# Kernel optimization log

Measured on AMD Instinct MI355X. Metric: run time of the kernel, lower is better.

Reference implementation:

```python
import jax, jax.numpy as jnp
import numpy as np

EPS = 1e-12  # matches torch F.normalize default eps

def _l2_normalize(v, axis=-1):
    n = jnp.sqrt(jnp.sum(v * v, axis=axis, keepdims=True))
    return v / jnp.maximum(n, EPS)

def setup_inputs() -> dict:
    key = jax.random.key(0)
    k1, k2, k3 = jax.random.split(key, 3)
    B, S, D_IN, D_OUT, T = 4, 4096, 1024, 1024, 1024
    std = 1.0 / np.sqrt(D_IN)
    return {
        "x": jax.random.normal(k1, (B, S, D_IN), dtype=jnp.float32),
        "key_tokens": jax.random.normal(k2, (T, D_IN), dtype=jnp.float32) * std,
        "value_tokens": jax.random.normal(k3, (T, D_OUT), dtype=jnp.float32) * std,
        "temp": jnp.ones((T, 1), dtype=jnp.float32),
    }

def reference(x, key_tokens, value_tokens, temp):
    # x: [B,S,D_in]; key_tokens: [T,D_in]; value_tokens: [T,D_out]; temp: [T,1]
    x_norm = _l2_normalize(x)                      # [B,S,D_in]
    k_norm = _l2_normalize(key_tokens)             # [T,D_in]
    sim = jnp.einsum('bsd,td->bst', x_norm, k_norm)  # [B,S,T]
    sim = sim * jax.nn.sigmoid(temp).reshape(1, 1, -1)
    # mod_softmax: scale each row to RMS-norm sqrt(T), then exact GELU
    T = sim.shape[-1]
    scale = jnp.sqrt(jnp.float32(T)) / jnp.sqrt(jnp.sum(sim * sim, axis=-1, keepdims=True))
    weights = jax.nn.gelu(sim * scale, approximate=False)  # [B,S,T]
    return jnp.einsum('bst,to->bso', weights, value_tokens)  # [B,S,D_out]
```

## Files before the change

### kernel.cpp

```cpp
#include <hip/hip_runtime.h>
#include <math.h>

typedef __attribute__((ext_vector_type(8))) short short8;
typedef __attribute__((ext_vector_type(4))) float floatx4;

__device__ __forceinline__ float bf2f(unsigned short u) {
    union { unsigned int u; float f; } v;
    v.u = ((unsigned int)u) << 16;
    return v.f;
}

__device__ __forceinline__ unsigned short f2bf(float f) {
    union { float f; unsigned int u; } v;
    v.f = f;
    unsigned int r = v.u + 0x7fffu + ((v.u >> 16) & 1u);
    return (unsigned short)(r >> 16);
}

__device__ __forceinline__ void gload16_lds(const void* g, void* l) {
    __builtin_amdgcn_global_load_lds(
        (const __attribute__((address_space(1))) unsigned int*)g,
        (__attribute__((address_space(3))) unsigned int*)l, 16, 0, 0);
}

__device__ __forceinline__ ushort4 cvt4(float4 v, float fa) {
    ushort4 o;
    o.x = f2bf(v.x * fa); o.y = f2bf(v.y * fa);
    o.z = f2bf(v.z * fa); o.w = f2bf(v.w * fa);
    return o;
}

__global__ __launch_bounds__(256) void prep_kernel(
    const float* __restrict__ x, const float* __restrict__ key,
    const float* __restrict__ temp, const float* __restrict__ val,
    unsigned short* __restrict__ xb, unsigned short* __restrict__ kf,
    unsigned short* __restrict__ VT, float* __restrict__ rowsq,
    int M, int T, int D, int Dout, int nRowBlocks) {
    const int bid = blockIdx.x;
    if (bid < nRowBlocks) {
        const int lane = threadIdx.x & 63;
        const int nWaves = nRowBlocks << 2;
        const int totRows = M + T;
        for (int row = (bid << 2) | (int)(threadIdx.x >> 6); row < totRows;
             row += nWaves) {
            const bool isx = row < M;
            const int r = isx ? row : row - M;
            const float4* s4 =
                (const float4*)(isx ? (x + (size_t)r * D) : (key + (size_t)r * D));
            float4 v0 = s4[lane];
            float4 v1 = s4[lane + 64];
            float4 v2 = s4[lane + 128];
            float4 v3 = s4[lane + 192];
            float s = v0.x * v0.x + v0.y * v0.y + v0.z * v0.z + v0.w * v0.w;
            s += v1.x * v1.x + v1.y * v1.y + v1.z * v1.z + v1.w * v1.w;
            s += v2.x * v2.x + v2.y * v2.y + v2.z * v2.z + v2.w * v2.w;
            s += v3.x * v3.x + v3.y * v3.y + v3.z * v3.z + v3.w * v3.w;
#pragma unroll
            for (int o = 32; o > 0; o >>= 1) s += __shfl_xor(s, o, 64);
            float fa = 1.0f / fmaxf(sqrtf(s), 1e-12f);
            if (isx) {
                if (lane == 0) rowsq[r] = 0.0f;
            } else {
                fa = fa / (1.0f + expf(-temp[r]));
            }
            ushort4* dst =
                (ushort4*)(isx ? (xb + (size_t)r * D) : (kf + (size_t)r * D));
            dst[lane] = cvt4(v0, fa);
            dst[lane + 64] = cvt4(v1, fa);
            dst[lane + 128] = cvt4(v2, fa);
            dst[lane + 192] = cvt4(v3, fa);
        }
    } else {
        __shared__ unsigned short tile[64][65];
        const int idx = bid - nRowBlocks;
        const int nCt = Dout >> 6;
        const int c0 = (idx % nCt) * 64;
        const int r0 = (idx / nCt) * 64;
        const int t = threadIdx.x;
        for (int i = t; i < 4096; i += 256) {
            int rr = i >> 6, cc = i & 63;
            tile[rr][cc] = f2bf(val[(size_t)(r0 + rr) * Dout + c0 + cc]);
        }
        __syncthreads();
        for (int i = t; i < 4096; i += 256) {
            int rr = i >> 6, cc = i & 63;
            VT[(size_t)(c0 + rr) * T + r0 + cc] = tile[cc][rr];
        }
    }
}

template <int MODE>
__global__ __launch_bounds__(256, 2) void gemm_pipe(
    const unsigned short* __restrict__ A, const unsigned short* __restrict__ B,
    void* __restrict__ Cv, float* __restrict__ rowsq, int M, int N, int K) {
    __shared__ __align__(16) char smem[73728];
    const int tid = threadIdx.x;
    const int lane = tid & 63;
    const int w = tid >> 6;
    const int wr = w >> 1;
    const int wc = w & 1;
    const int m0 = blockIdx.x * 256;
    const int n0 = blockIdx.y * 128;
    const int q = lane >> 4;
    const int cl = lane & 15;

    const int srow = lane >> 2;
    const int sch = (lane & 3) ^ ((lane & 32) >> 4);
    const unsigned short* gA = A + (size_t)(m0 + w * 16 + srow) * K + sch * 8;
    const unsigned short* gB = B + (size_t)(n0 + w * 16 + srow) * K + sch * 8;
    const unsigned short* rA0 = gA;
    const unsigned short* rA1 = gA + (size_t)64 * K;
    const unsigned short* rA2 = gA + (size_t)128 * K;
    const unsigned short* rA3 = gA + (size_t)192 * K;
    const unsigned short* rB0 = gB;
    const unsigned short* rB1 = gB + (size_t)64 * K;

    char* stA = smem + w * 1024;
    char* stB = stA + 16384;

    const int LB = ((cl * 64 + q * 16) ^ ((lane & 8) << 2));
    const char* rdA = (const char*)smem + LB + wr * 8192;
    const char* rdB = (const char*)smem + LB + 16384 + wc * 4096;

    floatx4 acc[8][4];
#pragma unroll
    for (int i = 0; i < 8; i++)
#pragma unroll
        for (int j = 0; j < 4; j++) acc[i][j] = (floatx4){0.f, 0.f, 0.f, 0.f};

    short8 af0[4], af1[4], bf0[4], bf1[4];

    gload16_lds(rA0, stA);
    gload16_lds(rA1, stA + 4096);
    gload16_lds(rB0, stB);
    gload16_lds(rA2, stA + 8192);
    gload16_lds(rA3, stA + 12288);
    gload16_lds(rB1, stB + 4096);
    gload16_lds(rA0 + 32, stA + 24576);
    gload16_lds(rA1 + 32, stA + 24576 + 4096);
    gload16_lds(rB0 + 32, stB + 24576);
    gload16_lds(rA2 + 32, stA + 24576 + 8192);
    gload16_lds(rA3 + 32, stA + 24576 + 12288);
    gload16_lds(rB1 + 32, stB + 24576 + 4096);
    asm volatile("s_waitcnt vmcnt(6)" ::: "memory");
    __builtin_amdgcn_s_barrier();
    rA0 += 64; rA1 += 64; rA2 += 64; rA3 += 64; rB0 += 64; rB1 += 64;

#define MFMA16(AF, BF, RO)                                                   \
    _Pragma("unroll") for (int mt = 0; mt < 4; ++mt)                         \
        _Pragma("unroll") for (int nt = 0; nt < 4; ++nt)                     \
            acc[RO + mt][nt] = __builtin_amdgcn_mfma_f32_16x16x32_bf16(      \
                AF[mt], BF[nt], acc[RO + mt][nt], 0, 0, 0);

#define TILE(SLOT, SSLOT, BF, KOFF)                                          \
    {                                                                        \
        BF[0] = *(const short8*)(rdB + SLOT * 24576);                        \
        BF[1] = *(const short8*)(rdB + SLOT * 24576 + 1024);                 \
        BF[2] = *(const short8*)(rdB + SLOT * 24576 + 2048);                 \
        BF[3] = *(const short8*)(rdB + SLOT * 24576 + 3072);                 \
        af0[0] = *(const short8*)(rdA + SLOT * 24576);                       \
        af0[1] = *(const short8*)(rdA + SLOT * 24576 + 1024);                \
        af0[2] = *(const short8*)(rdA + SLOT * 24576 + 2048);                \
        af0[3] = *(const short8*)(rdA + SLOT * 24576 + 3072);                \
        gload16_lds(rA0 + KOFF, stA + SSLOT * 24576);                        \
        gload16_lds(rA1 + KOFF, stA + SSLOT * 24576 + 4096);                 \
        gload16_lds(rB0 + KOFF, stB + SSLOT * 24576);                        \
        __builtin_amdgcn_s_barrier();                                        \
        asm volatile("s_waitcnt lgkmcnt(0)" ::: "memory");                   \
        __builtin_amdgcn_sched_barrier(0);                                   \
        __builtin_amdgcn_s_setprio(1);                                       \
        MFMA16(af0, BF, 0)                                                   \
        __builtin_amdgcn_s_setprio(0);                                       \
        __builtin_amdgcn_s_barrier();                                        \
        af1[0] = *(const short8*)(rdA + SLOT * 24576 + 4096);                \
        af1[1] = *(const short8*)(rdA + SLOT * 24576 + 5120);                \
        af1[2] = *(const short8*)(rdA + SLOT * 24576 + 6144);                \
        af1[3] = *(const short8*)(rdA + SLOT * 24576 + 7168);                \
        gload16_lds(rA2 + KOFF, stA + SSLOT * 24576 + 8192);                 \
        gload16_lds(rA3 + KOFF, stA + SSLOT * 24576 + 12288);                \
        gload16_lds(rB1 + KOFF, stB + SSLOT * 24576 + 4096);                 \
        asm volatile("s_waitcnt vmcnt(6)" ::: "memory");                     \
        __builtin_amdgcn_s_barrier();                                        \
        asm volatile("s_waitcnt lgkmcnt(0)" ::: "memory");                   \
        __builtin_amdgcn_sched_barrier(0);                                   \
        __builtin_amdgcn_s_setprio(1);                                       \
        MFMA16(af1, BF, 4)                                                   \
        __builtin_amdgcn_s_setprio(0);                                       \
        __builtin_amdgcn_s_barrier();                                        \
    }

#define TILE_TAIL(SLOT, BF, DRAIN)                                           \
    {                                                                        \
        BF[0] = *(const short8*)(rdB + SLOT * 24576);                        \
        BF[1] = *(const short8*)(rdB + SLOT * 24576 + 1024);                 \
        BF[2] = *(const short8*)(rdB + SLOT * 24576 + 2048);                 \
        BF[3] = *(const short8*)(rdB + SLOT * 24576 + 3072);                 \
        af0[0] = *(const short8*)(rdA + SLOT * 24576);                       \
        af0[1] = *(const short8*)(rdA + SLOT * 24576 + 1024);                \
        af0[2] = *(const short8*)(rdA + SLOT * 24576 + 2048);                \
        af0[3] = *(const short8*)(rdA + SLOT * 24576 + 3072);                \
        __builtin_amdgcn_s_barrier();                                        \
        asm volatile("s_waitcnt lgkmcnt(0)" ::: "memory");                   \
        __builtin_amdgcn_sched_barrier(0);                                   \
        __builtin_amdgcn_s_setprio(1);                                       \
        MFMA16(af0, BF, 0)                                                   \
        __builtin_amdgcn_s_setprio(0);                                       \
        __builtin_amdgcn_s_barrier();                                        \
        af1[0] = *(const short8*)(rdA + SLOT * 24576 + 4096);                \
        af1[1] = *(const short8*)(rdA + SLOT * 24576 + 5120);                \
        af1[2] = *(const short8*)(rdA + SLOT * 24576 + 6144);                \
        af1[3] = *(const short8*)(rdA + SLOT * 24576 + 7168);                \
        if (DRAIN) asm volatile("s_waitcnt vmcnt(0)" ::: "memory");          \
        __builtin_amdgcn_s_barrier();                                        \
        asm volatile("s_waitcnt lgkmcnt(0)" ::: "memory");                   \
        __builtin_amdgcn_sched_barrier(0);                                   \
        __builtin_amdgcn_s_setprio(1);                                       \
        MFMA16(af1, BF, 4)                                                   \
        __builtin_amdgcn_s_setprio(0);                                       \
        __builtin_amdgcn_s_barrier();                                        \
    }

    for (int g = 0; g < 5; ++g) {
        TILE(0, 2, bf0, 0)
        TILE(1, 0, bf1, 32)
        TILE(2, 1, bf0, 64)
        TILE(0, 2, bf1, 96)
        TILE(1, 0, bf0, 128)
        TILE(2, 1, bf1, 160)
        rA0 += 192; rA1 += 192; rA2 += 192; rA3 += 192;
        rB0 += 192; rB1 += 192;
    }
    TILE_TAIL(0, bf0, 1)
    TILE_TAIL(1, bf1, 0)

#undef TILE
#undef TILE_TAIL
#undef MFMA16

#pragma unroll
    for (int mt = 0; mt < 8; ++mt) {
#pragma unroll
        for (int r = 0; r < 4; ++r) {
            const int m = m0 + wr * 128 + mt * 16 + q * 4 + r;
            if (MODE == 0) {
                unsigned short* C = (unsigned short*)Cv;
                float ssq = 0.f;
#pragma unroll
                for (int nt = 0; nt < 4; ++nt) {
                    float v = acc[mt][nt][r];
                    ssq += v * v;
                    C[(size_t)m * N + n0 + wc * 64 + nt * 16 + cl] = f2bf(v);
                }
#pragma unroll
                for (int o = 1; o < 16; o <<= 1) ssq += __shfl_xor(ssq, o, 64);
                if (cl == 0) atomicAdd(&rowsq[m], ssq);
            } else {
                float* C = (float*)Cv;
#pragma unroll
                for (int nt = 0; nt < 4; ++nt)
                    C[(size_t)m * N + n0 + wc * 64 + nt * 16 + cl] =
                        acc[mt][nt][r];
            }
        }
    }
}

__global__ __launch_bounds__(256) void gelu_kernel(unsigned short* __restrict__ sim,
                                                   const float* __restrict__ rowsq,
                                                   int nVec, int t8shift,
                                                   float sqrtT) {
    const int stride = gridDim.x * blockDim.x;
    const float kk = 0.70710678118654752f;
    for (int i = blockIdx.x * blockDim.x + threadIdx.x; i < nVec; i += stride) {
        short8 v = *(const short8*)(sim + (size_t)i * 8);
        const int row = i >> t8shift;
        const float scale = sqrtT / fmaxf(sqrtf(rowsq[row]), 1e-30f);
        short8 o;
#pragma unroll
        for (int j = 0; j < 8; j++) {
            float z = bf2f((unsigned short)v[j]) * scale;
            o[j] = (short)f2bf(0.5f * z * (1.0f + erff(z * kk)));
        }
        *(short8*)(sim + (size_t)i * 8) = o;
    }
}

extern "C" void kernel_launch(void* const* d_in, const int* in_sizes, int n_in,
                              void* d_out, int out_size, void* d_ws, size_t ws_size,
                              hipStream_t stream) {
    const float* x    = (const float*)d_in[0];
    const float* key  = (const float*)d_in[1];
    const float* val  = (const float*)d_in[2];
    const float* temp = (const float*)d_in[3];
    float* out = (float*)d_out;

    const int T = in_sizes[3];
    const int D = in_sizes[1] / T;
    const int Dout = in_sizes[2] / T;
    const int M = in_sizes[0] / D;

    char* ws = (char*)d_ws;
    size_t off = 0;
    unsigned short* xb  = (unsigned short*)(ws + off); off += (size_t)M * D * 2;
    unsigned short* sim = (unsigned short*)(ws + off); off += (size_t)M * T * 2;
    unsigned short* kf  = (unsigned short*)(ws + off); off += (size_t)T * D * 2;
    unsigned short* VT  = (unsigned short*)(ws + off); off += (size_t)Dout * T * 2;
    float* rowsq = (float*)(ws + off); off += (size_t)M * 4;
    (void)ws_size; (void)n_in; (void)out_size;

    const int nTrTiles = (T >> 6) * (Dout >> 6);
    const int nRowBlocks = 1024;
    prep_kernel<<<nRowBlocks + nTrTiles, 256, 0, stream>>>(
        x, key, temp, val, xb, kf, VT, rowsq, M, T, D, Dout, nRowBlocks);
    gemm_pipe<0><<<dim3(M / 256, T / 128), 256, 0, stream>>>(xb, kf, sim, rowsq,
                                                             M, T, D);
    int t8shift = 0;
    {
        int t8 = T >> 3;
        while ((1 << t8shift) < t8) t8shift++;
    }
    gelu_kernel<<<2048, 256, 0, stream>>>(sim, rowsq, M * (T >> 3), t8shift,
                                          sqrtf((float)T));
    gemm_pipe<1><<<dim3(M / 256, Dout / 128), 256, 0, stream>>>(sim, VT, out,
                                                                nullptr, M, Dout, T);
}
```

Baseline: 218.3 us.

## Software-pipeline LDS fragment reads one K-tile ahead with double-buffered registers

Restructures the GEMM main loop so fragments for the next K-tile are read from LDS into a second register set while the MFMAs for the current tile run. Each tile now uses one barrier with a full vmcnt drain instead of four barriers, and partial lgkmcnt waits let LDS reads overlap the MFMAs. The cost is more live vector registers (six fragment arrays instead of four), which could lower occupancy or cause spills. Global loads now wait on vmcnt(0) each tile, so less global prefetch stays in flight.

```diff
diff --git a/kernel.cpp b/kernel.cpp
--- a/kernel.cpp
+++ b/kernel.cpp
@@ -128,22 +128,34 @@
 #pragma unroll
         for (int j = 0; j < 4; j++) acc[i][j] = (floatx4){0.f, 0.f, 0.f, 0.f};
 
-    short8 af0[4], af1[4], bf0[4], bf1[4];
+    short8 bfa[4], a0a[4], a1a[4], bfb[4], a0b[4], a1b[4];
 
     gload16_lds(rA0, stA);
     gload16_lds(rA1, stA + 4096);
-    gload16_lds(rB0, stB);
     gload16_lds(rA2, stA + 8192);
     gload16_lds(rA3, stA + 12288);
+    gload16_lds(rB0, stB);
     gload16_lds(rB1, stB + 4096);
     gload16_lds(rA0 + 32, stA + 24576);
     gload16_lds(rA1 + 32, stA + 24576 + 4096);
-    gload16_lds(rB0 + 32, stB + 24576);
     gload16_lds(rA2 + 32, stA + 24576 + 8192);
     gload16_lds(rA3 + 32, stA + 24576 + 12288);
+    gload16_lds(rB0 + 32, stB + 24576);
     gload16_lds(rB1 + 32, stB + 24576 + 4096);
-    asm volatile("s_waitcnt vmcnt(6)" ::: "memory");
+    asm volatile("s_waitcnt vmcnt(0)" ::: "memory");
     __builtin_amdgcn_s_barrier();
+    bfa[0] = *(const short8*)(rdB);
+    bfa[1] = *(const short8*)(rdB + 1024);
+    bfa[2] = *(const short8*)(rdB + 2048);
+    bfa[3] = *(const short8*)(rdB + 3072);
+    a0a[0] = *(const short8*)(rdA);
+    a0a[1] = *(const short8*)(rdA + 1024);
+    a0a[2] = *(const short8*)(rdA + 2048);
+    a0a[3] = *(const short8*)(rdA + 3072);
+    a1a[0] = *(const short8*)(rdA + 4096);
+    a1a[1] = *(const short8*)(rdA + 5120);
+    a1a[2] = *(const short8*)(rdA + 6144);
+    a1a[3] = *(const short8*)(rdA + 7168);
     rA0 += 64; rA1 += 64; rA2 += 64; rA3 += 64; rB0 += 64; rB1 += 64;
 
 #define MFMA16(AF, BF, RO)                                                   \
@@ -152,89 +164,103 @@
             acc[RO + mt][nt] = __builtin_amdgcn_mfma_f32_16x16x32_bf16(      \
                 AF[mt], BF[nt], acc[RO + mt][nt], 0, 0, 0);
 
-#define TILE(SLOT, SSLOT, BF, KOFF)                                          \
+#define TILE(RSLOT, SSLOT, KOFF, BFc, A0c, A1c, BFn, A0n, A1n)               \
     {                                                                        \
-        BF[0] = *(const short8*)(rdB + SLOT * 24576);                        \
-        BF[1] = *(const short8*)(rdB + SLOT * 24576 + 1024);                 \
-        BF[2] = *(const short8*)(rdB + SLOT * 24576 + 2048);                 \
-        BF[3] = *(const short8*)(rdB + SLOT * 24576 + 3072);                 \
-        af0[0] = *(const short8*)(rdA + SLOT * 24576);                       \
-        af0[1] = *(const short8*)(rdA + SLOT * 24576 + 1024);                \
-        af0[2] = *(const short8*)(rdA + SLOT * 24576 + 2048);                \
-        af0[3] = *(const short8*)(rdA + SLOT * 24576 + 3072);                \
+        asm volatile("s_waitcnt vmcnt(0)" ::: "memory");                     \
+        __builtin_amdgcn_sched_barrier(0);                                   \
+        __builtin_amdgcn_s_barrier();                                        \
         gload16_lds(rA0 + KOFF, stA + SSLOT * 24576);                        \
         gload16_lds(rA1 + KOFF, stA + SSLOT * 24576 + 4096);                 \
-        gload16_lds(rB0 + KOFF, stB + SSLOT * 24576);                        \
-        __builtin_amdgcn_s_barrier();                                        \
-        asm volatile("s_waitcnt lgkmcnt(0)" ::: "memory");                   \
-        __builtin_amdgcn_sched_barrier(0);                                   \
-        __builtin_amdgcn_s_setprio(1);                                       \
-        MFMA16(af0, BF, 0)                                                   \
-        __builtin_amdgcn_s_setprio(0);                                       \
-        __builtin_amdgcn_s_barrier();                                        \
-        af1[0] = *(const short8*)(rdA + SLOT * 24576 + 4096);                \
-        af1[1] = *(const short8*)(rdA + SLOT * 24576 + 5120);                \
-        af1[2] = *(const short8*)(rdA + SLOT * 24576 + 6144);                \
-        af1[3] = *(const short8*)(rdA + SLOT * 24576 + 7168);                \
         gload16_lds(rA2 + KOFF, stA + SSLOT * 24576 + 8192);                 \
         gload16_lds(rA3 + KOFF, stA + SSLOT * 24576 + 12288);                \
+        gload16_lds(rB0 + KOFF, stB + SSLOT * 24576);                        \
         gload16_lds(rB1 + KOFF, stB + SSLOT * 24576 + 4096);                 \
-        asm volatile("s_waitcnt vmcnt(6)" ::: "memory");                     \
+        asm volatile("s_waitcnt lgkmcnt(4)" ::: "memory");                   \
+        __builtin_amdgcn_sched_barrier(0);                                   \
+        __builtin_amdgcn_s_setprio(1);                                       \
+        MFMA16(A0c, BFc, 0)                                                  \
+        __builtin_amdgcn_s_setprio(0);                                       \
+        BFn[0] = *(const short8*)(rdB + RSLOT * 24576);                      \
+        BFn[1] = *(const short8*)(rdB + RSLOT * 24576 + 1024);               \
+        BFn[2] = *(const short8*)(rdB + RSLOT * 24576 + 2048);               \
+        BFn[3] = *(const short8*)(rdB + RSLOT * 24576 + 3072);               \
+        A0n[0] = *(const short8*)(rdA + RSLOT * 24576);                      \
+        A0n[1] = *(const short8*)(rdA + RSLOT * 24576 + 1024);               \
+        A0n[2] = *(const short8*)(rdA + RSLOT * 24576 + 2048);               \
+        A0n[3] = *(const short8*)(rdA + RSLOT * 24576 + 3072);               \
+        A1n[0] = *(const short8*)(rdA + RSLOT * 24576 + 4096);               \
+        A1n[1] = *(const short8*)(rdA + RSLOT * 24576 + 5120);               \
+        A1n[2] = *(const short8*)(rdA + RSLOT * 24576 + 6144);               \
+        A1n[3] = *(const short8*)(rdA + RSLOT * 24576 + 7168);               \
+        asm volatile("s_waitcnt lgkmcnt(12)" ::: "memory");                  \
+        __builtin_amdgcn_sched_barrier(0);                                   \
+        __builtin_amdgcn_s_setprio(1);                                       \
+        MFMA16(A1c, BFc, 4)                                                  \
+        __builtin_amdgcn_s_setprio(0);                                       \
+    }
+
+#define TILE_T30(RSLOT, BFc, A0c, A1c, BFn, A0n, A1n)                        \
+    {                                                                        \
+        asm volatile("s_waitcnt vmcnt(0)" ::: "memory");                     \
+        __builtin_amdgcn_sched_barrier(0);                                   \
         __builtin_amdgcn_s_barrier();                                        \
+        asm volatile("s_waitcnt lgkmcnt(4)" ::: "memory");                   \
+        __builtin_amdgcn_sched_barrier(0);                                   \
+        __builtin_amdgcn_s_setprio(1);                                       \
+        MFMA16(A0c, BFc, 0)                                                  \
+        __builtin_amdgcn_s_setprio(0);                                       \
+        BFn[0] = *(const short8*)(rdB + RSLOT * 24576);                      \
+        BFn[1] = *(const short8*)(rdB + RSLOT * 24576 + 1024);               \
+        BFn[2] = *(const short8*)(rdB + RSLOT * 24576 + 2048);               \
+        BFn[3] = *(const short8*)(rdB + RSLOT * 24576 + 3072);               \
+        A0n[0] = *(const short8*)(rdA + RSLOT * 24576);                      \
+        A0n[1] = *(const short8*)(rdA + RSLOT * 24576 + 1024);               \
+        A0n[2] = *(const short8*)(rdA + RSLOT * 24576 + 2048);               \
+        A0n[3] = *(const short8*)(rdA + RSLOT * 24576 + 3072);               \
+        A1n[0] = *(const short8*)(rdA + RSLOT * 24576 + 4096);               \
+        A1n[1] = *(const short8*)(rdA + RSLOT * 24576 + 5120);               \
+        A1n[2] = *(const short8*)(rdA + RSLOT * 24576 + 6144);               \
+        A1n[3] = *(const short8*)(rdA + RSLOT * 24576 + 7168);               \
+        asm volatile("s_waitcnt lgkmcnt(12)" ::: "memory");                  \
+        __builtin_amdgcn_sched_barrier(0);                                   \
+        __builtin_amdgcn_s_setprio(1);                                       \
+        MFMA16(A1c, BFc, 4)                                                  \
+        __builtin_amdgcn_s_setprio(0);                                       \
+    }
+
+#define TILE_T31(BFc, A0c, A1c)                                              \
+    {                                                                        \
+        asm volatile("s_waitcnt vmcnt(0)" ::: "memory");                     \
+        __builtin_amdgcn_sched_barrier(0);                                   \
+        __builtin_amdgcn_s_barrier();                                        \
+        asm volatile("s_waitcnt lgkmcnt(4)" ::: "memory");                   \
+        __builtin_amdgcn_sched_barrier(0);                                   \
+        __builtin_amdgcn_s_setprio(1);                                       \
+        MFMA16(A0c, BFc, 0)                                                  \
+        __builtin_amdgcn_s_setprio(0);                                       \
         asm volatile("s_waitcnt lgkmcnt(0)" ::: "memory");                   \
         __builtin_amdgcn_sched_barrier(0);                                   \
         __builtin_amdgcn_s_setprio(1);                                       \
-        MFMA16(af1, BF, 4)                                                   \
-        __builtin_amdgcn_s_setprio(0);                                       \
-        __builtin_amdgcn_s_barrier();                                        \
-    }
-
-#define TILE_TAIL(SLOT, BF, DRAIN)                                           \
-    {                                                                        \
-        BF[0] = *(const short8*)(rdB + SLOT * 24576);                        \
-        BF[1] = *(const short8*)(rdB + SLOT * 24576 + 1024);                 \
-        BF[2] = *(const short8*)(rdB + SLOT * 24576 + 2048);                 \
-        BF[3] = *(const short8*)(rdB + SLOT * 24576 + 3072);                 \
-        af0[0] = *(const short8*)(rdA + SLOT * 24576);                       \
-        af0[1] = *(const short8*)(rdA + SLOT * 24576 + 1024);                \
-        af0[2] = *(const short8*)(rdA + SLOT * 24576 + 2048);                \
-        af0[3] = *(const short8*)(rdA + SLOT * 24576 + 3072);                \
-        __builtin_amdgcn_s_barrier();                                        \
-        asm volatile("s_waitcnt lgkmcnt(0)" ::: "memory");                   \
-        __builtin_amdgcn_sched_barrier(0);                                   \
-        __builtin_amdgcn_s_setprio(1);                                       \
-        MFMA16(af0, BF, 0)                                                   \
-        __builtin_amdgcn_s_setprio(0);                                       \
-        __builtin_amdgcn_s_barrier();                                        \
-        af1[0] = *(const short8*)(rdA + SLOT * 24576 + 4096);                \
-        af1[1] = *(const short8*)(rdA + SLOT * 24576 + 5120);                \
-        af1[2] = *(const short8*)(rdA + SLOT * 24576 + 6144);                \
-        af1[3] = *(const short8*)(rdA + SLOT * 24576 + 7168);                \
-        if (DRAIN) asm volatile("s_waitcnt vmcnt(0)" ::: "memory");          \
-        __builtin_amdgcn_s_barrier();                                        \
-        asm volatile("s_waitcnt lgkmcnt(0)" ::: "memory");                   \
-        __builtin_amdgcn_sched_barrier(0);                                   \
-        __builtin_amdgcn_s_setprio(1);                                       \
-        MFMA16(af1, BF, 4)                                                   \
-        __builtin_amdgcn_s_setprio(0);                                       \
-        __builtin_amdgcn_s_barrier();                                        \
+        MFMA16(A1c, BFc, 4)                                                  \
+        __builtin_amdgcn_s_setprio(0);                                       \
     }
 
     for (int g = 0; g < 5; ++g) {
-        TILE(0, 2, bf0, 0)
-        TILE(1, 0, bf1, 32)
-        TILE(2, 1, bf0, 64)
-        TILE(0, 2, bf1, 96)
-        TILE(1, 0, bf0, 128)
-        TILE(2, 1, bf1, 160)
+        TILE(1, 2, 0,   bfa, a0a, a1a, bfb, a0b, a1b)
+        TILE(2, 0, 32,  bfb, a0b, a1b, bfa, a0a, a1a)
+        TILE(0, 1, 64,  bfa, a0a, a1a, bfb, a0b, a1b)
+        TILE(1, 2, 96,  bfb, a0b, a1b, bfa, a0a, a1a)
+        TILE(2, 0, 128, bfa, a0a, a1a, bfb, a0b, a1b)
+        TILE(0, 1, 160, bfb, a0b, a1b, bfa, a0a, a1a)
         rA0 += 192; rA1 += 192; rA2 += 192; rA3 += 192;
         rB0 += 192; rB1 += 192;
     }
-    TILE_TAIL(0, bf0, 1)
-    TILE_TAIL(1, bf1, 0)
+    TILE_T30(1, bfa, a0a, a1a, bfb, a0b, a1b)
+    TILE_T31(bfb, a0b, a1b)
 
 #undef TILE
-#undef TILE_TAIL
+#undef TILE_T30
+#undef TILE_T31
 #undef MFMA16
 
 #pragma unroll
```

Measured after the change: 226.3 us. +3.7%, slower.
